# Kernel optimization log

Measured on AMD Instinct MI355X. Metric: run time of the kernel, lower is better.

Reference implementation:

```python
import jax, jax.numpy as jnp
import numpy as np

N = 10000          # nodes
E = 160000         # edges (avg degree 16)
IN_DIM = 10
OUT_DIM = 3
EDGE_DIM = 9
HIDDEN = 256
HEADS = 8
C = HIDDEN // HEADS  # 32 per-head channels
T = 5
BN_EPS = 1e-5
LRELU_SLOPE = 0.2  # GATv2Conv negative_slope default


def setup_inputs() -> dict:
    key = jax.random.key(0)
    ks = jax.random.split(key, 16)
    g = lambda k, shape, scale: jax.random.normal(k, shape, dtype=jnp.float32) * scale
    s = 1.0 / np.sqrt(HIDDEN)
    inp = {}
    inp['x'] = g(ks[0], (N, IN_DIM), 1.0)
    inp['edge_attr'] = g(ks[1], (E, EDGE_DIM), 1.0)
    inp['edge_index'] = jax.random.randint(ks[2], (2, E), 0, N, dtype=jnp.int32)
    # lift
    inp['lift_W'] = g(ks[3], (IN_DIM, HIDDEN), 1.0 / np.sqrt(IN_DIM))
    inp['lift_b'] = jnp.zeros((HIDDEN,), jnp.float32)
    # T stacked GATv2 layers
    inp['Wl'] = g(ks[4], (T, HIDDEN, HIDDEN), s)
    inp['bl'] = jnp.zeros((T, HIDDEN), jnp.float32)
    inp['Wr'] = g(ks[5], (T, HIDDEN, HIDDEN), s)
    inp['br'] = jnp.zeros((T, HIDDEN), jnp.float32)
    inp['We'] = g(ks[6], (T, EDGE_DIM, HIDDEN), 1.0 / np.sqrt(EDGE_DIM))
    inp['att'] = g(ks[7], (T, HEADS, C), 1.0 / np.sqrt(C))
    inp['conv_bias'] = jnp.zeros((T, HIDDEN), jnp.float32)
    inp['bn_gamma'] = jnp.ones((T, HIDDEN), jnp.float32)
    inp['bn_beta'] = jnp.zeros((T, HIDDEN), jnp.float32)
    # projection MLP: Lin-BN-ReLU, Lin-BN-ReLU, Lin
    inp['p1_W'] = g(ks[8], (HIDDEN, HIDDEN), s)
    inp['p1_b'] = jnp.zeros((HIDDEN,), jnp.float32)
    inp['pbn1_g'] = jnp.ones((HIDDEN,), jnp.float32)
    inp['pbn1_b'] = jnp.zeros((HIDDEN,), jnp.float32)
    inp['p2_W'] = g(ks[9], (HIDDEN, HIDDEN), s)
    inp['p2_b'] = jnp.zeros((HIDDEN,), jnp.float32)
    inp['pbn2_g'] = jnp.ones((HIDDEN,), jnp.float32)
    inp['pbn2_b'] = jnp.zeros((HIDDEN,), jnp.float32)
    inp['p3_W'] = g(ks[10], (HIDDEN, OUT_DIM), s)
    inp['p3_b'] = jnp.zeros((OUT_DIM,), jnp.float32)
    return inp


def _bn(h, gamma, beta):
    # BatchNorm1d with batch statistics (biased variance), eps=1e-5
    mu = h.mean(axis=0)
    var = jnp.var(h, axis=0)
    return gamma * (h - mu) * jax.lax.rsqrt(var + BN_EPS) + beta


def _forward(x, edge_attr, edge_index, lift_W, lift_b, Wl, bl, Wr, br, We, att,
             conv_bias, bn_gamma, bn_beta, p1_W, p1_b, pbn1_g, pbn1_b,
             p2_W, p2_b, pbn2_g, pbn2_b, p3_W, p3_b):
    src = edge_index[0]  # message source j
    dst = edge_index[1]  # message target i (softmax segments)
    # per_graph_edge_norm on cols 0:9 (== full edge_dim), single graph (batch=None):
    # per-column z-score over all edges of the graph
    ea = (edge_attr - edge_attr.mean(axis=0)) / (edge_attr.std(axis=0) + 1e-8)
    h = jax.nn.relu(x @ lift_W + lift_b)  # [N, HIDDEN]
    for t in range(T):
        xl = (h @ Wl[t] + bl[t]).reshape(N, HEADS, C)   # source transform
        xr = (h @ Wr[t] + br[t]).reshape(N, HEADS, C)   # target transform
        xe = (ea @ We[t]).reshape(E, HEADS, C)          # edge transform
        # GATv2: attention logits from leaky-relu'd summed features
        e = jax.nn.leaky_relu(xl[src] + xr[dst] + xe, LRELU_SLOPE)  # [E,H,C]
        logits = jnp.einsum('ehc,hc->eh', e, att[t])                # [E,H]
        # segment softmax over destination nodes
        m = jax.ops.segment_max(logits, dst, num_segments=N)
        m = jnp.where(jnp.isfinite(m), m, 0.0)
        z = jnp.exp(logits - m[dst])
        denom = jax.ops.segment_sum(z, dst, num_segments=N)
        alpha = z / (denom[dst] + 1e-16)                             # [E,H]
        agg = jax.ops.segment_sum(alpha[:, :, None] * xl[src], dst, num_segments=N)
        out = agg.reshape(N, HIDDEN) + conv_bias[t]
        h = jax.nn.elu(_bn(out, bn_gamma[t], bn_beta[t]))
    h = jax.nn.relu(_bn(h @ p1_W + p1_b, pbn1_g, pbn1_b))
    h = jax.nn.relu(_bn(h @ p2_W + p2_b, pbn2_g, pbn2_b))
    return h @ p3_W + p3_b  # [N, OUT_DIM]


def reference(x, edge_attr, edge_index, lift_W, lift_b, Wl, bl, Wr, br, We, att,
              conv_bias, bn_gamma, bn_beta, p1_W, p1_b, pbn1_g, pbn1_b,
              p2_W, p2_b, pbn2_g, pbn2_b, p3_W, p3_b):
    return _forward(x, edge_attr, edge_index, lift_W, lift_b, Wl, bl, Wr, br, We, att,
                    conv_bias, bn_gamma, bn_beta, p1_W, p1_b, pbn1_g, pbn1_b,
                    p2_W, p2_b, pbn2_g, pbn2_b, p3_W, p3_b)
```

## Files before the change

kernel.cpp:

```cpp
#include <hip/hip_runtime.h>

#define Nn 10000
#define Ee 160000
#define HID 256
#define EDIM 9
#define INDIM 10
#define Tt 5

typedef _Float16 f16;
typedef _Float16 f16x8 __attribute__((ext_vector_type(8)));
typedef _Float16 f16x4 __attribute__((ext_vector_type(4)));
typedef float f32x4 __attribute__((ext_vector_type(4)));

__global__ __launch_bounds__(256) void colstats_kernel(const float* __restrict__ in,
                                                       float* __restrict__ cs) {
  float s[9], s2[9];
#pragma unroll
  for (int k = 0; k < 9; ++k) { s[k] = 0.f; s2[k] = 0.f; }
  for (int i = blockIdx.x * blockDim.x + threadIdx.x; i < Ee; i += gridDim.x * blockDim.x) {
#pragma unroll
    for (int k = 0; k < 9; ++k) {
      float v = in[i * 9 + k];
      s[k] += v; s2[k] += v * v;
    }
  }
#pragma unroll
  for (int k = 0; k < 9; ++k) {
    for (int off = 1; off < 64; off <<= 1) {
      s[k] += __shfl_xor(s[k], off);
      s2[k] += __shfl_xor(s2[k], off);
    }
  }
  if ((threadIdx.x & 63) == 0) {
#pragma unroll
    for (int k = 0; k < 9; ++k) {
      atomicAdd(&cs[k], s[k]);
      atomicAdd(&cs[16 + k], s2[k]);
    }
  }
}

__global__ __launch_bounds__(256) void lift_kernel(const float* __restrict__ x,
                                                   const float* __restrict__ W,
                                                   const float* __restrict__ b,
                                                   f16* __restrict__ hq) {
  __shared__ float xs[INDIM];
  int n = blockIdx.x, ch = threadIdx.x;
  if (ch < INDIM) xs[ch] = x[n * INDIM + ch];
  __syncthreads();
  float s = b[ch];
#pragma unroll
  for (int k = 0; k < INDIM; ++k) s += xs[k] * W[k * 256 + ch];
  hq[n * 256 + ch] = (f16)fmaxf(s, 0.f);
}

__global__ __launch_bounds__(256) void degree_kernel(const int* __restrict__ dst,
                                                     int* __restrict__ deg) {
  int e = blockIdx.x * 256 + threadIdx.x;
  if (e < Ee) atomicAdd(&deg[dst[e]], 1);
}

__global__ __launch_bounds__(1024) void scan_kernel(const int* __restrict__ deg,
                                                    int* __restrict__ rowptr,
                                                    int* __restrict__ cursor) {
  __shared__ int part[1024];
  int tid = threadIdx.x;
  const int CH = (Nn + 1023) / 1024;
  int start = tid * CH;
  int s = 0;
  for (int i = 0; i < CH; ++i) { int idx = start + i; if (idx < Nn) s += deg[idx]; }
  part[tid] = s;
  __syncthreads();
  for (int off = 1; off < 1024; off <<= 1) {
    int v = part[tid];
    int w = (tid >= off) ? part[tid - off] : 0;
    __syncthreads();
    part[tid] = v + w;
    __syncthreads();
  }
  int run = part[tid] - s;
  for (int i = 0; i < CH; ++i) {
    int idx = start + i;
    if (idx < Nn) { rowptr[idx] = run; cursor[idx] = run; run += deg[idx]; }
  }
  if (tid == 0) rowptr[Nn] = Ee;
}

__global__ __launch_bounds__(256) void fill_kernel(const int* __restrict__ dst,
                                                   int* __restrict__ cursor,
                                                   int* __restrict__ perm) {
  int e = blockIdx.x * 256 + threadIdx.x;
  if (e < Ee) {
    int pos = atomicAdd(&cursor[dst[e]], 1);
    perm[pos] = e;
  }
}

__global__ __launch_bounds__(256) void eaperm_kernel(const float* __restrict__ edge_attr,
                                                     const float* __restrict__ cs,
                                                     const int* __restrict__ perm,
                                                     const int* __restrict__ srcIn,
                                                     int* __restrict__ srcp,
                                                     float* __restrict__ eap) {
  int idx = blockIdx.x * 256 + threadIdx.x;
  if (idx >= Ee) return;
  int e = perm[idx];
  srcp[idx] = srcIn[e];
  const float* a = edge_attr + e * 9;
  float o[12];
#pragma unroll
  for (int k = 0; k < 9; ++k) {
    float mu = cs[k] * (1.f / Ee);
    float var = fmaxf(cs[16 + k] * (1.f / Ee) - mu * mu, 0.f);
    o[k] = (a[k] - mu) / (sqrtf(var) + 1e-8f);
  }
  o[9] = o[10] = o[11] = 0.f;
  float4 v0 = {o[0], o[1], o[2], o[3]};
  float4 v1 = {o[4], o[5], o[6], o[7]};
  float4 v2 = {o[8], o[9], o[10], o[11]};
  *(float4*)(eap + (size_t)idx * 12 + 0) = v0;
  *(float4*)(eap + (size_t)idx * 12 + 4) = v1;
  *(float4*)(eap + (size_t)idx * 12 + 8) = v2;
}

__global__ __launch_bounds__(256) void convert_kernel(const float* __restrict__ Wl,
                                                      const float* __restrict__ Wr,
                                                      const float* __restrict__ p1,
                                                      const float* __restrict__ p2,
                                                      f16* __restrict__ wt) {
  int nrow = blockIdx.x, s = blockIdx.y, k = threadIdx.x;
  const float* srcp; int n = nrow; size_t dst;
  if (s < 5) {
    dst = (size_t)s * 131072 + (size_t)nrow * 256 + k;
    if (nrow < 256) srcp = Wl + s * 65536;
    else { srcp = Wr + s * 65536; n = nrow - 256; }
  } else {
    if (nrow >= 256) return;
    dst = 655360 + (size_t)(s - 5) * 65536 + (size_t)nrow * 256 + k;
    srcp = (s == 5) ? p1 : p2;
  }
  wt[dst] = (f16)srcp[k * 256 + n];
}

__global__ __launch_bounds__(256) void prep_bias_kernel(const float* __restrict__ bl,
                                                        const float* __restrict__ br,
                                                        float* __restrict__ bc) {
  int idx = blockIdx.x * 256 + threadIdx.x;
  if (idx >= 2560) return;
  int t = idx >> 9, c = idx & 511;
  bc[idx] = (c < 256) ? bl[t * 256 + c] : br[t * 256 + c - 256];
}

__global__ __launch_bounds__(256) void gemm16_kernel(const f16* __restrict__ A,
                                                     const f16* __restrict__ BT,
                                                     const float* __restrict__ bias,
                                                     const float* __restrict__ sums,
                                                     const float* __restrict__ gamma,
                                                     const float* __restrict__ beta,
                                                     int act,
                                                     f16* __restrict__ out,
                                                     int M, int OS) {
  __shared__ __align__(16) f16 As[64][264];
  __shared__ __align__(16) f16 Bs[64][264];
  const int tid = threadIdx.x;
  const int wave = tid >> 6, lane = tid & 63;
  const int l15 = lane & 15, quad = lane >> 4;
  const int m0 = blockIdx.y * 64, n0 = blockIdx.x * 64;
  const int wm = (wave >> 1) * 32, wn = (wave & 1) * 32;
  const int colbase = (tid & 31) * 8, rowbase = tid >> 5;
  float sA[8], tA[8];
  if (act >= 0) {
#pragma unroll
    for (int c4 = 0; c4 < 2; ++c4) {
      float4 su = *(const float4*)(sums + colbase + c4 * 4);
      float4 sq = *(const float4*)(sums + 256 + colbase + c4 * 4);
      float4 g4 = *(const float4*)(gamma + colbase + c4 * 4);
      float4 b4 = *(const float4*)(beta + colbase + c4 * 4);
      float su_[4] = {su.x, su.y, su.z, su.w};
      float sq_[4] = {sq.x, sq.y, sq.z, sq.w};
      float g_[4] = {g4.x, g4.y, g4.z, g4.w};
      float b_[4] = {b4.x, b4.y, b4.z, b4.w};
#pragma unroll
      for (int c = 0; c < 4; ++c) {
        float mu = su_[c] * (1.f / Nn);
        float var = fmaxf(sq_[c] * (1.f / Nn) - mu * mu, 0.f);
        float is = rsqrtf(var + 1e-5f) * g_[c];
        sA[c4 * 4 + c] = is;
        tA[c4 * 4 + c] = b_[c] - mu * is;
      }
    }
  }
#pragma unroll
  for (int i = 0; i < 8; ++i) {
    int row = rowbase + 8 * i;
    f16x8 av = {};
    int gm = m0 + row;
    if (gm < M) av = *(const f16x8*)(A + (size_t)gm * 256 + colbase);
    if (act >= 0) {
#pragma unroll
      for (int e = 0; e < 8; ++e) {
        float y = (float)av[e] * sA[e] + tA[e];
        if (act == 0) y = y > 0.f ? y : (__expf(y) - 1.f);
        else y = fmaxf(y, 0.f);
        av[e] = (f16)y;
      }
    }
    *(f16x8*)(&As[row][colbase]) = av;
    f16x8 bv = *(const f16x8*)(BT + (size_t)(n0 + row) * 256 + colbase);
    *(f16x8*)(&Bs[row][colbase]) = bv;
  }
  __syncthreads();
  f32x4 zero4 = {0.f, 0.f, 0.f, 0.f};
  f32x4 acc[2][2] = {{zero4, zero4}, {zero4, zero4}};
#pragma unroll
  for (int kk = 0; kk < 256; kk += 32) {
    f16x8 a0 = *(const f16x8*)(&As[wm + l15][kk + quad * 8]);
    f16x8 a1 = *(const f16x8*)(&As[wm + 16 + l15][kk + quad * 8]);
    f16x8 b0 = *(const f16x8*)(&Bs[wn + l15][kk + quad * 8]);
    f16x8 b1 = *(const f16x8*)(&Bs[wn + 16 + l15][kk + quad * 8]);
    acc[0][0] = __builtin_amdgcn_mfma_f32_16x16x32_f16(a0, b0, acc[0][0], 0, 0, 0);
    acc[0][1] = __builtin_amdgcn_mfma_f32_16x16x32_f16(a0, b1, acc[0][1], 0, 0, 0);
    acc[1][0] = __builtin_amdgcn_mfma_f32_16x16x32_f16(a1, b0, acc[1][0], 0, 0, 0);
    acc[1][1] = __builtin_amdgcn_mfma_f32_16x16x32_f16(a1, b1, acc[1][1], 0, 0, 0);
  }
  __syncthreads();
  f16* Cs = (f16*)&As[0][0];
#pragma unroll
  for (int ni = 0; ni < 2; ++ni) {
    int nl = wn + ni * 16 + l15;
    float bv = bias[n0 + nl];
#pragma unroll
    for (int mi = 0; mi < 2; ++mi)
#pragma unroll
      for (int r = 0; r < 4; ++r)
        Cs[(wm + mi * 16 + quad * 4 + r) * 72 + nl] = (f16)(acc[mi][ni][r] + bv);
  }
  __syncthreads();
  {
    int row = tid >> 2, c4 = (tid & 3) * 16;
    int gm = m0 + row;
    if (gm < M) {
      f16x8 v0 = *(const f16x8*)(&Cs[row * 72 + c4]);
      f16x8 v1 = *(const f16x8*)(&Cs[row * 72 + c4 + 8]);
      *(f16x8*)(out + (size_t)gm * OS + n0 + c4) = v0;
      *(f16x8*)(out + (size_t)gm * OS + n0 + c4 + 8) = v1;
    }
  }
}

__global__ __launch_bounds__(256) void gat_fused(const f16* __restrict__ hxlr,
                                                 const float* __restrict__ eap,
                                                 const int* __restrict__ srcp,
                                                 const int* __restrict__ rowptr,
                                                 const float* __restrict__ We_t,
                                                 const float* __restrict__ att_t,
                                                 const float* __restrict__ cb_t,
                                                 f16* __restrict__ outb) {
  int wave = threadIdx.x >> 6, lane = threadIdx.x & 63;
  int i = blockIdx.x * 4 + wave;
  if (i >= Nn) return;
  int ch = lane * 4;
  float we[9][4];
#pragma unroll
  for (int k = 0; k < 9; ++k) {
    float4 w4 = *(const float4*)(We_t + k * 256 + ch);
    we[k][0] = w4.x; we[k][1] = w4.y; we[k][2] = w4.z; we[k][3] = w4.w;
  }
  float4 a4 = *(const float4*)(att_t + ch);
  float att[4] = {a4.x, a4.y, a4.z, a4.w};
  f16x4 xr4 = *(const f16x4*)(hxlr + (size_t)i * 512 + 256 + ch);
  float xri[4] = {(float)xr4[0], (float)xr4[1], (float)xr4[2], (float)xr4[3]};
  float acc[4] = {0.f, 0.f, 0.f, 0.f};
  float d = 0.f;
  int r0 = rowptr[i], r1 = rowptr[i + 1];
  for (int base = r0; base < r1; base += 4) {
    int cnt = r1 - base;
    int ib[4];
#pragma unroll
    for (int b = 0; b < 4; ++b) ib[b] = base + (b < cnt ? b : cnt - 1);
    int js[4];
#pragma unroll
    for (int b = 0; b < 4; ++b) js[b] = srcp[ib[b]];
    float xlv[4][4];
#pragma unroll
    for (int b = 0; b < 4; ++b) {
      f16x4 v4 = *(const f16x4*)(hxlr + (size_t)js[b] * 512 + ch);
      xlv[b][0] = (float)v4[0]; xlv[b][1] = (float)v4[1];
      xlv[b][2] = (float)v4[2]; xlv[b][3] = (float)v4[3];
    }
    float sp[4];
#pragma unroll
    for (int b = 0; b < 4; ++b) {
      const float* ep = eap + (size_t)ib[b] * 12;
      float4 e0 = *(const float4*)ep;
      float4 e1 = *(const float4*)(ep + 4);
      float e8 = ep[8];
      float s = 0.f;
#pragma unroll
      for (int c = 0; c < 4; ++c) {
        float v = xlv[b][c] + xri[c];
        v += e0.x * we[0][c] + e0.y * we[1][c] + e0.z * we[2][c] + e0.w * we[3][c];
        v += e1.x * we[4][c] + e1.y * we[5][c] + e1.z * we[6][c] + e1.w * we[7][c];
        v += e8 * we[8][c];
        v = v > 0.f ? v : 0.2f * v;
        s += att[c] * v;
      }
      sp[b] = s;
    }
#pragma unroll
    for (int b = 0; b < 4; ++b) {
      sp[b] += __shfl_xor(sp[b], 1);
      sp[b] += __shfl_xor(sp[b], 2);
      sp[b] += __shfl_xor(sp[b], 4);
    }
#pragma unroll
    for (int b = 0; b < 4; ++b) {
      float z = (b < cnt) ? __expf(fminf(sp[b], 75.f)) : 0.f;
      d += z;
#pragma unroll
      for (int c = 0; c < 4; ++c) acc[c] += z * xlv[b][c];
    }
  }
  float inv = 1.f / (d + 1e-16f);
  float4 cb4 = *(const float4*)(cb_t + ch);
  f16x4 o;
  o[0] = (f16)(acc[0] * inv + cb4.x);
  o[1] = (f16)(acc[1] * inv + cb4.y);
  o[2] = (f16)(acc[2] * inv + cb4.z);
  o[3] = (f16)(acc[3] * inv + cb4.w);
  *(f16x4*)(outb + (size_t)i * 256 + ch) = o;
}

__global__ __launch_bounds__(256) void bn_stats_kernel(const f16* __restrict__ v,
                                                       float* __restrict__ sums) {
  __shared__ float ls[512];
  int tid = threadIdx.x;
  for (int i = tid; i < 512; i += 256) ls[i] = 0.f;
  __syncthreads();
  int wave = tid >> 6, lane = tid & 63, ch = lane * 4;
  float s[4] = {0.f, 0.f, 0.f, 0.f}, s2[4] = {0.f, 0.f, 0.f, 0.f};
  for (int r = blockIdx.x * 4 + wave; r < Nn; r += gridDim.x * 4) {
    f16x4 x4 = *(const f16x4*)(v + (size_t)r * 256 + ch);
#pragma unroll
    for (int c = 0; c < 4; ++c) {
      float x = (float)x4[c];
      s[c] += x; s2[c] += x * x;
    }
  }
#pragma unroll
  for (int c = 0; c < 4; ++c) {
    atomicAdd(&ls[ch + c], s[c]);
    atomicAdd(&ls[256 + ch + c], s2[c]);
  }
  __syncthreads();
  for (int i = tid; i < 512; i += 256) atomicAdd(&sums[i], ls[i]);
}

__global__ __launch_bounds__(256) void final_kernel(const f16* __restrict__ hq,
                                                    const float* __restrict__ sums,
                                                    const float* __restrict__ gamma,
                                                    const float* __restrict__ beta,
                                                    const float* __restrict__ W,
                                                    const float* __restrict__ b,
                                                    float* __restrict__ out3) {
  int wave = threadIdx.x >> 6, lane = threadIdx.x & 63;
  int n = blockIdx.x * 4 + wave;
  if (n >= Nn) return;
  int ch = lane * 4;
  float4 su = *(const float4*)(sums + ch);
  float4 sq = *(const float4*)(sums + 256 + ch);
  float4 g4 = *(const float4*)(gamma + ch);
  float4 b4 = *(const float4*)(beta + ch);
  float su_[4] = {su.x, su.y, su.z, su.w};
  float sq_[4] = {sq.x, sq.y, sq.z, sq.w};
  float g_[4] = {g4.x, g4.y, g4.z, g4.w};
  float bb_[4] = {b4.x, b4.y, b4.z, b4.w};
  f16x4 h4 = *(const f16x4*)(hq + (size_t)n * 256 + ch);
  float s0 = 0.f, s1 = 0.f, s2 = 0.f;
#pragma unroll
  for (int c = 0; c < 4; ++c) {
    float mu = su_[c] * (1.f / Nn);
    float var = fmaxf(sq_[c] * (1.f / Nn) - mu * mu, 0.f);
    float is = rsqrtf(var + 1e-5f) * g_[c];
    float y = fmaxf(((float)h4[c] - mu) * is + bb_[c], 0.f);
    const float* w = W + (ch + c) * 3;
    s0 += y * w[0]; s1 += y * w[1]; s2 += y * w[2];
  }
  for (int off = 1; off < 64; off <<= 1) {
    s0 += __shfl_xor(s0, off);
    s1 += __shfl_xor(s1, off);
    s2 += __shfl_xor(s2, off);
  }
  if (lane == 0) {
    out3[n * 3 + 0] = s0 + b[0];
    out3[n * 3 + 1] = s1 + b[1];
    out3[n * 3 + 2] = s2 + b[2];
  }
}

extern "C" void kernel_launch(void* const* d_in, const int* in_sizes, int n_in,
                              void* d_out, int out_size, void* d_ws, size_t ws_size,
                              hipStream_t stream) {
  const float* x         = (const float*)d_in[0];
  const float* edge_attr = (const float*)d_in[1];
  const int*   eidx      = (const int*)d_in[2];
  const float* lift_W    = (const float*)d_in[3];
  const float* lift_b    = (const float*)d_in[4];
  const float* Wl        = (const float*)d_in[5];
  const float* bl        = (const float*)d_in[6];
  const float* Wr        = (const float*)d_in[7];
  const float* br        = (const float*)d_in[8];
  const float* We        = (const float*)d_in[9];
  const float* att       = (const float*)d_in[10];
  const float* conv_b    = (const float*)d_in[11];
  const float* bn_g      = (const float*)d_in[12];
  const float* bn_b      = (const float*)d_in[13];
  const float* p1_W      = (const float*)d_in[14];
  const float* p1_b      = (const float*)d_in[15];
  const float* pbn1_g    = (const float*)d_in[16];
  const float* pbn1_b    = (const float*)d_in[17];
  const float* p2_W      = (const float*)d_in[18];
  const float* p2_b      = (const float*)d_in[19];
  const float* pbn2_g    = (const float*)d_in[20];
  const float* pbn2_b    = (const float*)d_in[21];
  const float* p3_W      = (const float*)d_in[22];
  const float* p3_b      = (const float*)d_in[23];
  const int* srcI = eidx;
  const int* dstI = eidx + Ee;

  char* wp = (char*)d_ws;
  auto carve = [&](size_t bytes) -> void* {
    void* p = (void*)wp;
    wp += (bytes + 255) & ~(size_t)255;
    return p;
  };
  float* eap    = (float*)carve((size_t)Ee * 12 * sizeof(float));
  f16*   h16    = (f16*)carve((size_t)Nn * 256 * sizeof(f16));
  f16*   w16t   = (f16*)carve((size_t)786432 * sizeof(f16));
  float* biascat= (float*)carve((size_t)2560 * sizeof(float));
  f16*   hxlr   = (f16*)carve((size_t)Nn * 512 * sizeof(f16));
  f16*   outb16 = (f16*)carve((size_t)Nn * 256 * sizeof(f16));
  int*   deg    = (int*)carve((size_t)Nn * sizeof(int));
  int*   rowptr = (int*)carve((size_t)(Nn + 1) * sizeof(int));
  int*   cursor = (int*)carve((size_t)Nn * sizeof(int));
  int*   perm   = (int*)carve((size_t)Ee * sizeof(int));
  int*   srcp   = (int*)carve((size_t)Ee * sizeof(int));
  float* cstats = (float*)carve(32 * sizeof(float));
  float* bnsA   = (float*)carve((size_t)7 * 512 * sizeof(float));

  hipMemsetAsync(cstats, 0, 32 * sizeof(float), stream);
  hipMemsetAsync(deg, 0, Nn * sizeof(int), stream);
  hipMemsetAsync(bnsA, 0, (size_t)7 * 512 * sizeof(float), stream);

  colstats_kernel<<<64, 256, 0, stream>>>(edge_attr, cstats);
  lift_kernel<<<Nn, 256, 0, stream>>>(x, lift_W, lift_b, h16);
  degree_kernel<<<(Ee + 255) / 256, 256, 0, stream>>>(dstI, deg);
  scan_kernel<<<1, 1024, 0, stream>>>(deg, rowptr, cursor);
  fill_kernel<<<(Ee + 255) / 256, 256, 0, stream>>>(dstI, cursor, perm);
  eaperm_kernel<<<(Ee + 255) / 256, 256, 0, stream>>>(edge_attr, cstats, perm, srcI, srcp, eap);
  convert_kernel<<<dim3(512, 7), 256, 0, stream>>>(Wl, Wr, p1_W, p2_W, w16t);
  prep_bias_kernel<<<10, 256, 0, stream>>>(bl, br, biascat);

  const int MB = (Nn + 63) / 64;
  for (int t = 0; t < Tt; ++t) {
    const f16* Ain = (t == 0) ? h16 : outb16;
    const float* sums = (t == 0) ? nullptr : bnsA + (size_t)(t - 1) * 512;
    int act = (t == 0) ? -1 : 0;
    gemm16_kernel<<<dim3(8, MB), 256, 0, stream>>>(Ain, w16t + (size_t)t * 131072,
                                                   biascat + t * 512, sums,
                                                   bn_g + (t > 0 ? (t - 1) * 256 : 0),
                                                   bn_b + (t > 0 ? (t - 1) * 256 : 0),
                                                   act, hxlr, Nn, 512);
    gat_fused<<<2500, 256, 0, stream>>>(hxlr, eap, srcp, rowptr,
                                        We + t * 9 * 256, att + t * 256,
                                        conv_b + t * 256, outb16);
    bn_stats_kernel<<<128, 256, 0, stream>>>(outb16, bnsA + (size_t)t * 512);
  }
  f16* pA = hxlr;
  f16* pB = hxlr + (size_t)Nn * 256;
  gemm16_kernel<<<dim3(4, MB), 256, 0, stream>>>(outb16, w16t + 655360, p1_b,
                                                 bnsA + 4 * 512, bn_g + 4 * 256, bn_b + 4 * 256,
                                                 0, pA, Nn, 256);
  bn_stats_kernel<<<128, 256, 0, stream>>>(pA, bnsA + 5 * 512);
  gemm16_kernel<<<dim3(4, MB), 256, 0, stream>>>(pA, w16t + 720896, p2_b,
                                                 bnsA + 5 * 512, pbn1_g, pbn1_b,
                                                 1, pB, Nn, 256);
  bn_stats_kernel<<<128, 256, 0, stream>>>(pB, bnsA + 6 * 512);
  final_kernel<<<2500, 256, 0, stream>>>(pB, bnsA + 6 * 512, pbn2_g, pbn2_b, p3_W, p3_b,
                                         (float*)d_out);
}
```

Baseline: 623.0 us.

## Fuse prep kernels, BN stats into GEMM/GAT, and use fp16 edge math

Merges the colstats/degree, fill/eaperm and convert/bias prep kernels, removing the perm indirection and several launches. BatchNorm column statistics now accumulate inside gat_fused and the projection GEMMs, so the separate bn_stats passes go away. Edge attributes are stored as padded fp16 and the GATv2 edge projection runs in packed half arithmetic, which cuts bandwidth but lowers precision. Uses readfirstlane for wave-uniform indices and a single memset for all zeroed buffers; per-block LDS atomics add some contention.

```diff
diff --git a/kernel.cpp b/kernel.cpp
--- a/kernel.cpp
+++ b/kernel.cpp
@@ -12,8 +12,15 @@
 typedef _Float16 f16x4 __attribute__((ext_vector_type(4)));
 typedef float f32x4 __attribute__((ext_vector_type(4)));
 
-__global__ __launch_bounds__(256) void colstats_kernel(const float* __restrict__ in,
-                                                       float* __restrict__ cs) {
+static __device__ __forceinline__ f16x4 splat4(f16 x) {
+  f16x4 r = {x, x, x, x};
+  return r;
+}
+
+__global__ __launch_bounds__(256) void prep1_kernel(const float* __restrict__ in,
+                                                    const int* __restrict__ dst,
+                                                    float* __restrict__ cs,
+                                                    int* __restrict__ deg) {
   float s[9], s2[9];
 #pragma unroll
   for (int k = 0; k < 9; ++k) { s[k] = 0.f; s2[k] = 0.f; }
@@ -23,6 +30,7 @@
       float v = in[i * 9 + k];
       s[k] += v; s2[k] += v * v;
     }
+    atomicAdd(&deg[dst[i]], 1);
   }
 #pragma unroll
   for (int k = 0; k < 9; ++k) {
@@ -52,12 +60,6 @@
 #pragma unroll
   for (int k = 0; k < INDIM; ++k) s += xs[k] * W[k * 256 + ch];
   hq[n * 256 + ch] = (f16)fmaxf(s, 0.f);
-}
-
-__global__ __launch_bounds__(256) void degree_kernel(const int* __restrict__ dst,
-                                                     int* __restrict__ deg) {
-  int e = blockIdx.x * 256 + threadIdx.x;
-  if (e < Ee) atomicAdd(&deg[dst[e]], 1);
 }
 
 __global__ __launch_bounds__(1024) void scan_kernel(const int* __restrict__ deg,
@@ -86,49 +88,51 @@
   if (tid == 0) rowptr[Nn] = Ee;
 }
 
-__global__ __launch_bounds__(256) void fill_kernel(const int* __restrict__ dst,
-                                                   int* __restrict__ cursor,
-                                                   int* __restrict__ perm) {
+__global__ __launch_bounds__(256) void fill_eaperm_kernel(const float* __restrict__ edge_attr,
+                                                          const float* __restrict__ cs,
+                                                          const int* __restrict__ srcIn,
+                                                          const int* __restrict__ dstIn,
+                                                          int* __restrict__ cursor,
+                                                          int* __restrict__ srcp,
+                                                          f16* __restrict__ eap16) {
   int e = blockIdx.x * 256 + threadIdx.x;
-  if (e < Ee) {
-    int pos = atomicAdd(&cursor[dst[e]], 1);
-    perm[pos] = e;
-  }
-}
-
-__global__ __launch_bounds__(256) void eaperm_kernel(const float* __restrict__ edge_attr,
-                                                     const float* __restrict__ cs,
-                                                     const int* __restrict__ perm,
-                                                     const int* __restrict__ srcIn,
-                                                     int* __restrict__ srcp,
-                                                     float* __restrict__ eap) {
-  int idx = blockIdx.x * 256 + threadIdx.x;
-  if (idx >= Ee) return;
-  int e = perm[idx];
-  srcp[idx] = srcIn[e];
+  if (e >= Ee) return;
+  int pos = atomicAdd(&cursor[dstIn[e]], 1);
+  srcp[pos] = srcIn[e];
   const float* a = edge_attr + e * 9;
-  float o[12];
+  f16 o[16];
 #pragma unroll
   for (int k = 0; k < 9; ++k) {
     float mu = cs[k] * (1.f / Ee);
     float var = fmaxf(cs[16 + k] * (1.f / Ee) - mu * mu, 0.f);
-    o[k] = (a[k] - mu) / (sqrtf(var) + 1e-8f);
-  }
-  o[9] = o[10] = o[11] = 0.f;
-  float4 v0 = {o[0], o[1], o[2], o[3]};
-  float4 v1 = {o[4], o[5], o[6], o[7]};
-  float4 v2 = {o[8], o[9], o[10], o[11]};
-  *(float4*)(eap + (size_t)idx * 12 + 0) = v0;
-  *(float4*)(eap + (size_t)idx * 12 + 4) = v1;
-  *(float4*)(eap + (size_t)idx * 12 + 8) = v2;
+    o[k] = (f16)((a[k] - mu) / (sqrtf(var) + 1e-8f));
+  }
+#pragma unroll
+  for (int k = 9; k < 16; ++k) o[k] = (f16)0.f;
+  f16x8 v0, v1;
+#pragma unroll
+  for (int k = 0; k < 8; ++k) { v0[k] = o[k]; v1[k] = o[8 + k]; }
+  *(f16x8*)(eap16 + (size_t)pos * 16) = v0;
+  *(f16x8*)(eap16 + (size_t)pos * 16 + 8) = v1;
 }
 
 __global__ __launch_bounds__(256) void convert_kernel(const float* __restrict__ Wl,
                                                       const float* __restrict__ Wr,
                                                       const float* __restrict__ p1,
                                                       const float* __restrict__ p2,
-                                                      f16* __restrict__ wt) {
+                                                      const float* __restrict__ bl,
+                                                      const float* __restrict__ br,
+                                                      f16* __restrict__ wt,
+                                                      float* __restrict__ biascat) {
   int nrow = blockIdx.x, s = blockIdx.y, k = threadIdx.x;
+  if (s == 7) {
+    int flat = nrow * 256 + k;
+    if (flat < 2560) {
+      int t = flat >> 9, c = flat & 511;
+      biascat[flat] = (c < 256) ? bl[t * 256 + c] : br[t * 256 + c - 256];
+    }
+    return;
+  }
   const float* srcp; int n = nrow; size_t dst;
   if (s < 5) {
     dst = (size_t)s * 131072 + (size_t)nrow * 256 + k;
@@ -142,15 +146,6 @@
   wt[dst] = (f16)srcp[k * 256 + n];
 }
 
-__global__ __launch_bounds__(256) void prep_bias_kernel(const float* __restrict__ bl,
-                                                        const float* __restrict__ br,
-                                                        float* __restrict__ bc) {
-  int idx = blockIdx.x * 256 + threadIdx.x;
-  if (idx >= 2560) return;
-  int t = idx >> 9, c = idx & 511;
-  bc[idx] = (c < 256) ? bl[t * 256 + c] : br[t * 256 + c - 256];
-}
-
 __global__ __launch_bounds__(256) void gemm16_kernel(const f16* __restrict__ A,
                                                      const f16* __restrict__ BT,
                                                      const float* __restrict__ bias,
@@ -159,7 +154,8 @@
                                                      const float* __restrict__ beta,
                                                      int act,
                                                      f16* __restrict__ out,
-                                                     int M, int OS) {
+                                                     int M, int OS,
+                                                     float* __restrict__ statsout) {
   __shared__ __align__(16) f16 As[64][264];
   __shared__ __align__(16) f16 Bs[64][264];
   const int tid = threadIdx.x;
@@ -246,33 +242,49 @@
       *(f16x8*)(out + (size_t)gm * OS + n0 + c4 + 8) = v1;
     }
   }
+  if (statsout && tid < 64) {
+    int col = tid;
+    float s = 0.f, s2 = 0.f;
+    int rmax = (M - m0 < 64) ? (M - m0) : 64;
+    for (int r = 0; r < rmax; ++r) {
+      float xv = (float)Cs[r * 72 + col];
+      s += xv; s2 += xv * xv;
+    }
+    atomicAdd(&statsout[n0 + col], s);
+    atomicAdd(&statsout[256 + n0 + col], s2);
+  }
 }
 
 __global__ __launch_bounds__(256) void gat_fused(const f16* __restrict__ hxlr,
-                                                 const float* __restrict__ eap,
+                                                 const f16* __restrict__ eap16,
                                                  const int* __restrict__ srcp,
                                                  const int* __restrict__ rowptr,
                                                  const float* __restrict__ We_t,
                                                  const float* __restrict__ att_t,
                                                  const float* __restrict__ cb_t,
-                                                 f16* __restrict__ outb) {
-  int wave = threadIdx.x >> 6, lane = threadIdx.x & 63;
-  int i = blockIdx.x * 4 + wave;
-  if (i >= Nn) return;
+                                                 f16* __restrict__ outb,
+                                                 float* __restrict__ bns) {
+  __shared__ float ls[512];
+  const int tid = threadIdx.x;
+  for (int q = tid; q < 512; q += 256) ls[q] = 0.f;
+  __syncthreads();
+  int wave = tid >> 6, lane = tid & 63;
+  int i = __builtin_amdgcn_readfirstlane(blockIdx.x * 4 + wave);
   int ch = lane * 4;
-  float we[9][4];
+  f16x4 we16[9];
 #pragma unroll
   for (int k = 0; k < 9; ++k) {
     float4 w4 = *(const float4*)(We_t + k * 256 + ch);
-    we[k][0] = w4.x; we[k][1] = w4.y; we[k][2] = w4.z; we[k][3] = w4.w;
+    we16[k][0] = (f16)w4.x; we16[k][1] = (f16)w4.y;
+    we16[k][2] = (f16)w4.z; we16[k][3] = (f16)w4.w;
   }
   float4 a4 = *(const float4*)(att_t + ch);
   float att[4] = {a4.x, a4.y, a4.z, a4.w};
   f16x4 xr4 = *(const f16x4*)(hxlr + (size_t)i * 512 + 256 + ch);
-  float xri[4] = {(float)xr4[0], (float)xr4[1], (float)xr4[2], (float)xr4[3]};
   float acc[4] = {0.f, 0.f, 0.f, 0.f};
   float d = 0.f;
-  int r0 = rowptr[i], r1 = rowptr[i + 1];
+  int r0 = __builtin_amdgcn_readfirstlane(rowptr[i]);
+  int r1 = __builtin_amdgcn_readfirstlane(rowptr[i + 1]);
   for (int base = r0; base < r1; base += 4) {
     int cnt = r1 - base;
     int ib[4];
@@ -281,29 +293,26 @@
     int js[4];
 #pragma unroll
     for (int b = 0; b < 4; ++b) js[b] = srcp[ib[b]];
-    float xlv[4][4];
+    f16x4 xl4[4];
+#pragma unroll
+    for (int b = 0; b < 4; ++b)
+      xl4[b] = *(const f16x4*)(hxlr + (size_t)js[b] * 512 + ch);
+    float sp[4];
 #pragma unroll
     for (int b = 0; b < 4; ++b) {
-      f16x4 v4 = *(const f16x4*)(hxlr + (size_t)js[b] * 512 + ch);
-      xlv[b][0] = (float)v4[0]; xlv[b][1] = (float)v4[1];
-      xlv[b][2] = (float)v4[2]; xlv[b][3] = (float)v4[3];
-    }
-    float sp[4];
-#pragma unroll
-    for (int b = 0; b < 4; ++b) {
-      const float* ep = eap + (size_t)ib[b] * 12;
-      float4 e0 = *(const float4*)ep;
-      float4 e1 = *(const float4*)(ep + 4);
-      float e8 = ep[8];
+      const f16* ep = eap16 + (size_t)ib[b] * 16;
+      f16x8 ea = *(const f16x8*)ep;
+      f16 ea8 = ep[8];
+      f16x4 v = xl4[b] + xr4;
+#pragma unroll
+      for (int k = 0; k < 8; ++k) v += we16[k] * splat4(ea[k]);
+      v += we16[8] * splat4(ea8);
       float s = 0.f;
 #pragma unroll
       for (int c = 0; c < 4; ++c) {
-        float v = xlv[b][c] + xri[c];
-        v += e0.x * we[0][c] + e0.y * we[1][c] + e0.z * we[2][c] + e0.w * we[3][c];
-        v += e1.x * we[4][c] + e1.y * we[5][c] + e1.z * we[6][c] + e1.w * we[7][c];
-        v += e8 * we[8][c];
-        v = v > 0.f ? v : 0.2f * v;
-        s += att[c] * v;
+        float vf = (float)v[c];
+        vf = vf > 0.f ? vf : 0.2f * vf;
+        s += att[c] * vf;
       }
       sp[b] = s;
     }
@@ -318,42 +327,28 @@
       float z = (b < cnt) ? __expf(fminf(sp[b], 75.f)) : 0.f;
       d += z;
 #pragma unroll
-      for (int c = 0; c < 4; ++c) acc[c] += z * xlv[b][c];
+      for (int c = 0; c < 4; ++c) acc[c] += z * (float)xl4[b][c];
     }
   }
   float inv = 1.f / (d + 1e-16f);
   float4 cb4 = *(const float4*)(cb_t + ch);
   f16x4 o;
-  o[0] = (f16)(acc[0] * inv + cb4.x);
-  o[1] = (f16)(acc[1] * inv + cb4.y);
-  o[2] = (f16)(acc[2] * inv + cb4.z);
-  o[3] = (f16)(acc[3] * inv + cb4.w);
+  float ov[4];
+  ov[0] = acc[0] * inv + cb4.x;
+  ov[1] = acc[1] * inv + cb4.y;
+  ov[2] = acc[2] * inv + cb4.z;
+  ov[3] = acc[3] * inv + cb4.w;
+#pragma unroll
+  for (int c = 0; c < 4; ++c) o[c] = (f16)ov[c];
   *(f16x4*)(outb + (size_t)i * 256 + ch) = o;
-}
-
-__global__ __launch_bounds__(256) void bn_stats_kernel(const f16* __restrict__ v,
-                                                       float* __restrict__ sums) {
-  __shared__ float ls[512];
-  int tid = threadIdx.x;
-  for (int i = tid; i < 512; i += 256) ls[i] = 0.f;
-  __syncthreads();
-  int wave = tid >> 6, lane = tid & 63, ch = lane * 4;
-  float s[4] = {0.f, 0.f, 0.f, 0.f}, s2[4] = {0.f, 0.f, 0.f, 0.f};
-  for (int r = blockIdx.x * 4 + wave; r < Nn; r += gridDim.x * 4) {
-    f16x4 x4 = *(const f16x4*)(v + (size_t)r * 256 + ch);
-#pragma unroll
-    for (int c = 0; c < 4; ++c) {
-      float x = (float)x4[c];
-      s[c] += x; s2[c] += x * x;
-    }
-  }
 #pragma unroll
   for (int c = 0; c < 4; ++c) {
-    atomicAdd(&ls[ch + c], s[c]);
-    atomicAdd(&ls[256 + ch + c], s2[c]);
-  }
-  __syncthreads();
-  for (int i = tid; i < 512; i += 256) atomicAdd(&sums[i], ls[i]);
+    float xv = (float)o[c];
+    atomicAdd(&ls[ch + c], xv);
+    atomicAdd(&ls[256 + ch + c], xv * xv);
+  }
+  __syncthreads();
+  for (int q = tid; q < 512; q += 256) atomicAdd(&bns[q], ls[q]);
 }
 
 __global__ __launch_bounds__(256) void final_kernel(const f16* __restrict__ hq,
@@ -434,32 +429,28 @@
     wp += (bytes + 255) & ~(size_t)255;
     return p;
   };
-  float* eap    = (float*)carve((size_t)Ee * 12 * sizeof(float));
+  char*  zr     = (char*)carve((size_t)(32 + 7 * 512 + Nn) * 4);
+  float* cstats = (float*)zr;
+  float* bnsA   = (float*)(zr + 32 * 4);
+  int*   deg    = (int*)(zr + (32 + 7 * 512) * 4);
+  f16*   eap16  = (f16*)carve((size_t)Ee * 16 * sizeof(f16));
   f16*   h16    = (f16*)carve((size_t)Nn * 256 * sizeof(f16));
   f16*   w16t   = (f16*)carve((size_t)786432 * sizeof(f16));
   float* biascat= (float*)carve((size_t)2560 * sizeof(float));
   f16*   hxlr   = (f16*)carve((size_t)Nn * 512 * sizeof(f16));
   f16*   outb16 = (f16*)carve((size_t)Nn * 256 * sizeof(f16));
-  int*   deg    = (int*)carve((size_t)Nn * sizeof(int));
   int*   rowptr = (int*)carve((size_t)(Nn + 1) * sizeof(int));
   int*   cursor = (int*)carve((size_t)Nn * sizeof(int));
-  int*   perm   = (int*)carve((size_t)Ee * sizeof(int));
   int*   srcp   = (int*)carve((size_t)Ee * sizeof(int));
-  float* cstats = (float*)carve(32 * sizeof(float));
-  float* bnsA   = (float*)carve((size_t)7 * 512 * sizeof(float));
-
-  hipMemsetAsync(cstats, 0, 32 * sizeof(float), stream);
-  hipMemsetAsync(deg, 0, Nn * sizeof(int), stream);
-  hipMemsetAsync(bnsA, 0, (size_t)7 * 512 * sizeof(float), stream);
-
-  colstats_kernel<<<64, 256, 0, stream>>>(edge_attr, cstats);
+
+  hipMemsetAsync(zr, 0, (size_t)(32 + 7 * 512 + Nn) * 4, stream);
+
+  prep1_kernel<<<256, 256, 0, stream>>>(edge_attr, dstI, cstats, deg);
   lift_kernel<<<Nn, 256, 0, stream>>>(x, lift_W, lift_b, h16);
-  degree_kernel<<<(Ee + 255) / 256, 256, 0, stream>>>(dstI, deg);
   scan_kernel<<<1, 1024, 0, stream>>>(deg, rowptr, cursor);
-  fill_kernel<<<(Ee + 255) / 256, 256, 0, stream>>>(dstI, cursor, perm);
-  eaperm_kernel<<<(Ee + 255) / 256, 256, 0, stream>>>(edge_attr, cstats, perm, srcI, srcp, eap);
-  convert_kernel<<<dim3(512, 7), 256, 0, stream>>>(Wl, Wr, p1_W, p2_W, w16t);
-  prep_bias_kernel<<<10, 256, 0, stream>>>(bl, br, biascat);
+  fill_eaperm_kernel<<<(Ee + 255) / 256, 256, 0, stream>>>(edge_attr, cstats, srcI, dstI,
+                                                           cursor, srcp, eap16);
+  convert_kernel<<<dim3(512, 8), 256, 0, stream>>>(Wl, Wr, p1_W, p2_W, bl, br, w16t, biascat);
 
   const int MB = (Nn + 63) / 64;
   for (int t = 0; t < Tt; ++t) {
@@ -470,22 +461,20 @@
                                                    biascat + t * 512, sums,
                                                    bn_g + (t > 0 ? (t - 1) * 256 : 0),
                                                    bn_b + (t > 0 ? (t - 1) * 256 : 0),
-                                                   act, hxlr, Nn, 512);
-    gat_fused<<<2500, 256, 0, stream>>>(hxlr, eap, srcp, rowptr,
+                                                   act, hxlr, Nn, 512, nullptr);
+    gat_fused<<<2500, 256, 0, stream>>>(hxlr, eap16, srcp, rowptr,
                                         We + t * 9 * 256, att + t * 256,
-                                        conv_b + t * 256, outb16);
-    bn_stats_kernel<<<128, 256, 0, stream>>>(outb16, bnsA + (size_t)t * 512);
+                                        conv_b + t * 256, outb16,
+                                        bnsA + (size_t)t * 512);
   }
   f16* pA = hxlr;
   f16* pB = hxlr + (size_t)Nn * 256;
   gemm16_kernel<<<dim3(4, MB), 256, 0, stream>>>(outb16, w16t + 655360, p1_b,
                                                  bnsA + 4 * 512, bn_g + 4 * 256, bn_b + 4 * 256,
-                                                 0, pA, Nn, 256);
-  bn_stats_kernel<<<128, 256, 0, stream>>>(pA, bnsA + 5 * 512);
+                                                 0, pA, Nn, 256, bnsA + 5 * 512);
   gemm16_kernel<<<dim3(4, MB), 256, 0, stream>>>(pA, w16t + 720896, p2_b,
                                                  bnsA + 5 * 512, pbn1_g, pbn1_b,
-                                                 1, pB, Nn, 256);
-  bn_stats_kernel<<<128, 256, 0, stream>>>(pB, bnsA + 6 * 512);
+                                                 1, pB, Nn, 256, bnsA + 6 * 512);
   final_kernel<<<2500, 256, 0, stream>>>(pB, bnsA + 6 * 512, pbn2_g, pbn2_b, p3_W, p3_b,
                                          (float*)d_out);
 }
```

New measurement: 824.9 us. 32.4% more time.
